# Kernel optimization log

Hardware: AMD Instinct MI355X
Metric: run time of the kernel (lower is better)

The kernel has to match this reference:

```python
import jax, jax.numpy as jnp
import numpy as np

B, C, H, W = 8, 512, 64, 64
TEMB = 512
HIDDEN = 1024  # int(C * prompt_hidden_ratio=2.0)
K = C // 2     # max(1, int(C * topk_ratio=0.5))


def silu(x):
    return x * jax.nn.sigmoid(x)


def conv1x1(h, w, b):
    # h: [b,c,hh,ww], w: [out,in], b: [out]
    return jnp.einsum('bchw,oc->bohw', h, w) + b[None, :, None, None]


def setup_inputs() -> dict:
    key = jax.random.key(0)
    ks = jax.random.split(key, 12)
    s = 0.02  # small init so softmax/attention stay well-conditioned
    return {
        'x': jax.random.normal(ks[0], (B, C, H, W), jnp.float32),
        'temb': jax.random.normal(ks[1], (B, TEMB), jnp.float32),
        'w_affine': jax.random.normal(ks[2], (2 * C, TEMB), jnp.float32) * s,
        'b_affine': jnp.zeros((2 * C,), jnp.float32),
        'w_tp': jax.random.normal(ks[3], (C, TEMB), jnp.float32) * s,
        'b_tp': jnp.zeros((C,), jnp.float32),
        'w_m1': jax.random.normal(ks[4], (HIDDEN, 2 * C), jnp.float32) * s,
        'b_m1': jnp.zeros((HIDDEN,), jnp.float32),
        'w_m2': jax.random.normal(ks[5], (C, HIDDEN), jnp.float32) * s,
        'b_m2': jnp.zeros((C,), jnp.float32),
        'wq': jax.random.normal(ks[6], (C, C), jnp.float32) * s,
        'bq': jnp.zeros((C,), jnp.float32),
        'wk': jax.random.normal(ks[7], (C, C), jnp.float32) * s,
        'bk': jnp.zeros((C,), jnp.float32),
        'wv': jax.random.normal(ks[8], (C, C), jnp.float32) * s,
        'bv': jnp.zeros((C,), jnp.float32),
        'wo': jax.random.normal(ks[9], (C, C), jnp.float32) * s,
        'bo': jnp.zeros((C,), jnp.float32),
    }


def reference(x, temb, w_affine, b_affine, w_tp, b_tp, w_m1, b_m1, w_m2, b_m2,
              wq, bq, wk, bk, wv, bv, wo, bo):
    b, c, hgt, wgt = x.shape
    hw = hgt * wgt

    # TimeScaleShift
    temb_act = silu(temb)
    ss = temb_act @ w_affine.T + b_affine              # [b, 2c]
    scale, shift = jnp.split(ss, 2, axis=1)
    h = x * (1.0 + scale[:, :, None, None]) + shift[:, :, None, None]

    # channel prompt
    gap = h.mean(axis=(2, 3))                          # [b, c]
    time_prompt = temb_act @ w_tp.T + b_tp             # [b, c]
    pm = jnp.concatenate([gap, time_prompt], axis=1)   # [b, 2c]
    prompt = silu(pm @ w_m1.T + b_m1) @ w_m2.T + b_m2  # [b, c]

    # top-k channel selection
    _, topk_idx = jax.lax.top_k(prompt, K)             # [b, K] int32

    # q/k/v 1x1 convs, then gather selected channels
    qf = conv1x1(h, wq, bq).reshape(b, c, hw)
    kf = conv1x1(h, wk, bk).reshape(b, c, hw)
    vf = conv1x1(h, wv, bv).reshape(b, c, hw)
    idx3 = topk_idx[:, :, None]
    q = jnp.take_along_axis(qf, idx3, axis=1)          # [b, K, hw]
    k_feat = jnp.take_along_axis(kf, idx3, axis=1)
    v = jnp.take_along_axis(vf, idx3, axis=1)

    # channel attention on the selected subset
    attn = jnp.einsum('bkn,bln->bkl', q, k_feat) * (K ** -0.5)  # [b, K, K]
    attn = jax.nn.softmax(attn, axis=2)
    out = jnp.einsum('bkl,bln->bkn', attn, v)                   # [b, K, hw]

    # scatter back into a zero tensor at the selected channels
    out_full = jax.vmap(
        lambda o, i: jnp.zeros((c, hw), o.dtype).at[i].set(o)
    )(out, topk_idx).reshape(b, c, hgt, wgt)

    return conv1x1(out_full, wo, bo)
```

## Files before the change

kernel.cpp:

```cpp
#include <hip/hip_runtime.h>
#include <hip/hip_bf16.h>
#include <math.h>

typedef __hip_bfloat16 bf16;
typedef __bf16 bf16x8 __attribute__((ext_vector_type(8)));
typedef float f32x4 __attribute__((ext_vector_type(4)));

static __device__ __forceinline__ float b2f(bf16 v) { return __bfloat162float(v); }
static __device__ __forceinline__ bf16 f2b(float v) { return __float2bfloat16(v); }

#define GLOAD16(g, l) __builtin_amdgcn_global_load_lds( \
    (const __attribute__((address_space(1))) void*)(g), \
    (__attribute__((address_space(3))) void*)(l), 16, 0, 0)

template <typename TOUT, int KSL>
__global__ __launch_bounds__(256) void gemm_ws(
    const bf16* __restrict__ A, size_t sA, int lda,
    const bf16* __restrict__ Bt, size_t sB, int ldb,
    const float* __restrict__ bias, size_t sBias, int hasBias,
    TOUT* __restrict__ D, size_t sD, size_t sDs,
    int N, int NMT, int NNC)
{
    constexpr int KSTEPS = KSL / 32;
    const int id = blockIdx.x;
    const int bz = id & 7;
    int slot = id >> 3;
    const int mt = slot % NMT; slot /= NMT;
    const int nc = slot % NNC;
    const int ks = slot / NNC;
    const int n0 = nc * 256;

    A  += (size_t)bz * sA + (size_t)(mt * 32) * lda + (size_t)ks * KSL;
    Bt += (size_t)bz * sB + (size_t)ks * KSL;
    D  += (size_t)bz * sD + (size_t)ks * sDs;
    if (hasBias) bias += (size_t)bz * sBias + mt * 32;

    const int t = threadIdx.x, wv = t >> 6, lane = t & 63;
    const int lr = lane & 15, quad = lane >> 4;
    const int xr7 = lr & 7;

    __shared__ bf16 lA[32 * KSL];

    if constexpr (KSL == 512) {
#pragma unroll
        for (int rr = 0; rr < 8; ++rr) {
            const int r = wv * 8 + rr;
            GLOAD16(A + (size_t)r * lda + ((lane ^ (r & 7)) << 3), &lA[r * 512]);
        }
    } else {
#pragma unroll
        for (int rr = 0; rr < 4; ++rr) {
            const int rb = wv * 8 + rr * 2;
            const int rl = rb + (lane >> 5);
            GLOAD16(A + (size_t)rl * lda + (((lane & 31) ^ (rl & 7)) << 3),
                    &lA[rb * 256]);
        }
    }
    __syncthreads();

    f32x4 acc[2][4];
#pragma unroll
    for (int i = 0; i < 2; ++i)
#pragma unroll
        for (int j = 0; j < 4; ++j) acc[i][j] = (f32x4){0.f, 0.f, 0.f, 0.f};

    const bf16* bp[4];
#pragma unroll
    for (int j = 0; j < 4; ++j)
        bp[j] = Bt + (size_t)(n0 + wv * 64 + j * 16 + lr) * ldb + quad * 8;

#pragma unroll 2
    for (int k2 = 0; k2 < KSTEPS; ++k2) {
        const int ao = ((((k2 << 2) | quad) ^ xr7) << 3);
        bf16x8 bfr[4];
#pragma unroll
        for (int j = 0; j < 4; ++j)
            bfr[j] = *(const bf16x8*)(bp[j] + k2 * 32);
        bf16x8 af0 = *(const bf16x8*)&lA[lr * KSL + ao];
        bf16x8 af1 = *(const bf16x8*)&lA[(16 + lr) * KSL + ao];
#pragma unroll
        for (int j = 0; j < 4; ++j) {
            acc[0][j] = __builtin_amdgcn_mfma_f32_16x16x32_bf16(af0, bfr[j], acc[0][j], 0, 0, 0);
            acc[1][j] = __builtin_amdgcn_mfma_f32_16x16x32_bf16(af1, bfr[j], acc[1][j], 0, 0, 0);
        }
    }

#pragma unroll
    for (int i = 0; i < 2; ++i) {
#pragma unroll
        for (int r = 0; r < 4; ++r) {
            const int ml = i * 16 + quad * 4 + r;
            const int mrow = mt * 32 + ml;
            const float bvv = hasBias ? bias[ml] : 0.f;
#pragma unroll
            for (int j = 0; j < 4; ++j) {
                const int nn = n0 + wv * 64 + j * 16 + lr;
                const float v = acc[i][j][r] + bvv;
                if constexpr (__is_same(TOUT, float)) D[(size_t)mrow * N + nn] = v;
                else                                  D[(size_t)mrow * N + nn] = f2b(v);
            }
        }
    }
}

__global__ __launch_bounds__(512, 4) void gemm_qkv3(
    const bf16* __restrict__ Aall, const bf16* __restrict__ xT,
    const float* __restrict__ bias,
    bf16* __restrict__ qb, bf16* __restrict__ kb, bf16* __restrict__ vT)
{
    const int id = blockIdx.x;
    const int b = id & 7;
    const int slot = id >> 3;
    const int mt = slot % 12;
    const int n0 = (slot / 12) * 512;

    const bf16* A  = Aall + (size_t)b * 393216 + (size_t)(mt * 64) * 512;
    const bf16* Bt = xT + (size_t)b * 2097152;
    bias += b * 768 + mt * 64;

    const int t = threadIdx.x, w = t >> 6, lane = t & 63;
    const int lr = lane & 15, quad = lane >> 4;
    const int xr7 = lr & 7;

    __shared__ bf16 lA[64 * 512];

#pragma unroll
    for (int rr = 0; rr < 8; ++rr) {
        const int r = w * 8 + rr;
        GLOAD16(A + (size_t)r * 512 + ((lane ^ (r & 7)) << 3), &lA[r * 512]);
    }
    __syncthreads();

    f32x4 acc[4][4];
#pragma unroll
    for (int i = 0; i < 4; ++i)
#pragma unroll
        for (int j = 0; j < 4; ++j) acc[i][j] = (f32x4){0.f, 0.f, 0.f, 0.f};

    const bf16* bp0 = Bt + (size_t)(n0 + w * 64 + lr) * 512 + quad * 8;

    for (int k2 = 0; k2 < 16; ++k2) {
        const int ao = ((((k2 << 2) | quad) ^ xr7) << 3);
        bf16x8 bfr[4];
#pragma unroll
        for (int j = 0; j < 4; ++j)
            bfr[j] = *(const bf16x8*)(bp0 + (size_t)j * 8192 + k2 * 32);
        bf16x8 af[4];
#pragma unroll
        for (int i = 0; i < 4; ++i)
            af[i] = *(const bf16x8*)&lA[(i * 16 + lr) * 512 + ao];
#pragma unroll
        for (int i = 0; i < 4; ++i)
#pragma unroll
            for (int j = 0; j < 4; ++j)
                acc[i][j] = __builtin_amdgcn_mfma_f32_16x16x32_bf16(af[i], bfr[j], acc[i][j], 0, 0, 0);
    }

#pragma unroll
    for (int i = 0; i < 4; ++i) {
#pragma unroll
        for (int r = 0; r < 4; ++r) {
            const int ml = i * 16 + quad * 4 + r;
            const int mmg = mt * 64 + ml;
            const int mloc = mmg & 255;
            const float bvv = bias[ml];
#pragma unroll
            for (int j = 0; j < 4; ++j) {
                const int nn = n0 + w * 64 + j * 16 + lr;
                const float v = acc[i][j][r] + bvv;
                if (mt < 4)       qb[(size_t)b * 1048576 + (size_t)mloc * 4096 + nn] = f2b(v);
                else if (mt < 8)  kb[(size_t)b * 1048576 + (size_t)mloc * 4096 + nn] = f2b(v);
                else              vT[(size_t)b * 1048576 + (size_t)nn * 256 + mloc] = f2b(v);
            }
        }
    }
}

__global__ __launch_bounds__(256) void k_prep(const float* __restrict__ x,
                                              bf16* __restrict__ xT,
                                              float* __restrict__ xsump)
{
    const int b = blockIdx.z;
    const int c0 = blockIdx.y * 64;
    const int n0 = blockIdx.x * 512;
    const int t = threadIdx.x;
    const int cr = t >> 2;
    const int sub = t & 3;
    __shared__ bf16 tile[64][72];

    const float* xrow = x + ((size_t)b * 512 + c0 + cr) * 4096 + n0 + sub * 16;
    float s = 0.f;

    for (int st = 0; st < 8; ++st) {
        __syncthreads();
        float4 f[4];
#pragma unroll
        for (int q = 0; q < 4; ++q) f[q] = *(const float4*)(xrow + st * 64 + q * 4);
#pragma unroll
        for (int q = 0; q < 4; ++q) {
            s += f[q].x + f[q].y + f[q].z + f[q].w;
            union { bf16 h[4]; uint2 u; } p;
            p.h[0] = f2b(f[q].x); p.h[1] = f2b(f[q].y);
            p.h[2] = f2b(f[q].z); p.h[3] = f2b(f[q].w);
            *(uint2*)&tile[cr][sub * 16 + q * 4] = p.u;
        }
        __syncthreads();
        union { bf16 h[8]; uint4 u; } o0, o1;
#pragma unroll
        for (int i = 0; i < 8; ++i) o0.h[i] = tile[sub * 16 + i][cr];
#pragma unroll
        for (int i = 0; i < 8; ++i) o1.h[i] = tile[sub * 16 + 8 + i][cr];
        bf16* orow = xT + ((size_t)b * 4096 + n0 + st * 64 + cr) * 512 + c0 + sub * 16;
        *(uint4*)(orow)     = o0.u;
        *(uint4*)(orow + 8) = o1.u;
    }
    s += __shfl_down(s, 2);
    s += __shfl_down(s, 1);
    if (sub == 0) xsump[(size_t)blockIdx.x * 4096 + b * 512 + c0 + cr] = s;
}


__global__ void k_smallgemm(const float* __restrict__ in, const float* __restrict__ W,
                            const float* __restrict__ bias, float* __restrict__ out,
                            int Mrows, int O, int Kd, int act, int inAct)
{
    const int gw = (blockIdx.x * 256 + threadIdx.x) >> 6;
    const int lane = threadIdx.x & 63;
    if (gw >= Mrows * O) return;
    const int m = gw / O, o = gw - m * O;
    float s = 0.f;
    for (int k = lane; k < Kd; k += 64) {
        float iv = in[m * Kd + k];
        if (inAct) iv = iv / (1.f + expf(-iv));
        s += iv * W[(size_t)o * Kd + k];
    }
    for (int off = 32; off; off >>= 1) s += __shfl_down(s, off);
    if (lane == 0) {
        s += bias[o];
        if (act) s = s / (1.f + expf(-s));
        out[m * O + o] = s;
    }
}

__global__ void k_mlp1(const float* __restrict__ ss, const float* __restrict__ xsump,
                       const float* __restrict__ tp, const float* __restrict__ w_m1,
                       const float* __restrict__ b_m1, float* __restrict__ hidden)
{
    const int gw = (blockIdx.x * 256 + threadIdx.x) >> 6;
    const int lane = threadIdx.x & 63;
    if (gw >= 8 * 1024) return;
    const int m = gw >> 10, o = gw & 1023;
    float s = 0.f;
    for (int k = lane; k < 1024; k += 64) {
        float pv;
        if (k < 512) {
            float xs = 0.f;
#pragma unroll
            for (int p = 0; p < 8; ++p) xs += xsump[p * 4096 + m * 512 + k];
            pv = (1.f + ss[m * 1024 + k]) * (xs * (1.f / 4096.f))
                 + ss[m * 1024 + 512 + k];
        } else {
            pv = tp[m * 512 + k - 512];
        }
        s += pv * w_m1[(size_t)o * 1024 + k];
    }
    for (int off = 32; off; off >>= 1) s += __shfl_down(s, off);
    if (lane == 0) {
        s += b_m1[o];
        hidden[m * 1024 + o] = s / (1.f + expf(-s));
    }
}

__global__ void k_topk(const float* __restrict__ prompt, int* __restrict__ idx)
{
    __shared__ float v[512];
    __shared__ int sel[512];
    const int b = blockIdx.x, c = threadIdx.x;
    v[c] = prompt[b * 512 + c];
    __syncthreads();
    const float mv = v[c];
    int rank = 0;
    for (int j = 0; j < 512; ++j) {
        float o = v[j];
        rank += (o > mv) || (o == mv && j < c);
    }
    sel[c] = (rank < 256) ? 1 : 0;
    __syncthreads();
    if (rank < 256) {
        int pos = 0;
        for (int j = 0; j < c; ++j) pos += sel[j];
        idx[b * 256 + pos] = c;
    }
}

__global__ void k_gather(const int* __restrict__ idx, const float* __restrict__ ss,
                         const float* __restrict__ wq, const float* __restrict__ wk,
                         const float* __restrict__ wv, const float* __restrict__ wo,
                         bf16* __restrict__ wqkv_g, bf16* __restrict__ wo_g)
{
    const int b = blockIdx.z;
    const int* id = idx + b * 256;
    const int tid = blockIdx.x * 256 + threadIdx.x;
    {
        const int mat = tid >> 17, r = tid & 131071;
        const int j = r >> 9, c = r & 511;
        const int ch = id[j];
        const float* W = mat == 0 ? wq : (mat == 1 ? wk : wv);
        wqkv_g[(size_t)b * 393216 + tid] = f2b(W[ch * 512 + c] * (1.f + ss[b * 1024 + c]));
    }
    if (tid < 131072) {
        const int o = tid >> 8, j = tid & 255;
        wo_g[(size_t)b * 131072 + tid] = f2b(wo[o * 512 + id[j]]);
    }
}

__global__ void k_biasadj(const int* __restrict__ idx, const float* __restrict__ ss,
                          const float* __restrict__ wq, const float* __restrict__ bq,
                          const float* __restrict__ wk, const float* __restrict__ bk,
                          const float* __restrict__ wv, const float* __restrict__ bv,
                          float* __restrict__ bqkv)
{
    const int gw = (blockIdx.x * 256 + threadIdx.x) >> 6;
    const int lane = threadIdx.x & 63;
    if (gw >= 8 * 768) return;
    const int b = gw / 768, j3 = gw - b * 768;
    const int mat = j3 >> 8, j = j3 & 255;
    const int ch = idx[b * 256 + j];
    const float* W  = mat == 0 ? wq : (mat == 1 ? wk : wv);
    const float* Bb = mat == 0 ? bq : (mat == 1 ? bk : bv);
    const float* shift = ss + b * 1024 + 512;
    float s = 0.f;
    for (int c = lane; c < 512; c += 64)
        s += W[(size_t)ch * 512 + c] * shift[c];
    for (int off = 32; off; off >>= 1) s += __shfl_down(s, off);
    if (lane == 0) bqkv[b * 768 + j3] = Bb[ch] + s;
}

__global__ void k_softmax_red(const float* __restrict__ part, bf16* __restrict__ Pt)
{
    const int row = blockIdx.x;
    const int b = row >> 8, j = row & 255;
    const int t = threadIdx.x;
    const int lane = t & 63, wv = t >> 6;
    __shared__ float redm[4], reds[4];
    float v = 0.f;
#pragma unroll
    for (int s = 0; s < 8; ++s)
        v += part[((size_t)(s * 8 + b) * 256 + j) * 256 + t];
    v *= 0.0625f;
    float m = v;
    for (int off = 32; off; off >>= 1) m = fmaxf(m, __shfl_down(m, off));
    if (lane == 0) redm[wv] = m;
    __syncthreads();
    m = fmaxf(fmaxf(redm[0], redm[1]), fmaxf(redm[2], redm[3]));
    const float e = __expf(v - m);
    float s = e;
    for (int off = 32; off; off >>= 1) s += __shfl_down(s, off);
    if (lane == 0) reds[wv] = s;
    __syncthreads();
    s = reds[0] + reds[1] + reds[2] + reds[3];
    Pt[(size_t)b * 65536 + (size_t)t * 256 + j] = f2b(e / s);
}


extern "C" void kernel_launch(void* const* d_in, const int* in_sizes, int n_in,
                              void* d_out, int out_size, void* d_ws, size_t ws_size,
                              hipStream_t stream)
{
    const float* x        = (const float*)d_in[0];
    const float* temb     = (const float*)d_in[1];
    const float* w_affine = (const float*)d_in[2];
    const float* b_affine = (const float*)d_in[3];
    const float* w_tp     = (const float*)d_in[4];
    const float* b_tp     = (const float*)d_in[5];
    const float* w_m1     = (const float*)d_in[6];
    const float* b_m1     = (const float*)d_in[7];
    const float* w_m2     = (const float*)d_in[8];
    const float* b_m2     = (const float*)d_in[9];
    const float* wq       = (const float*)d_in[10];
    const float* bq       = (const float*)d_in[11];
    const float* wk       = (const float*)d_in[12];
    const float* bk       = (const float*)d_in[13];
    const float* wv       = (const float*)d_in[14];
    const float* bv       = (const float*)d_in[15];
    const float* wo       = (const float*)d_in[16];
    const float* bo       = (const float*)d_in[17];
    float* out = (float*)d_out;

    char* ws = (char*)d_ws;
    size_t off = 0;
    auto alloc = [&](size_t bytes) -> char* {
        char* p = ws + off;
        off += (bytes + 255) & ~(size_t)255;
        return p;
    };

    float* ssb      = (float*)alloc(8192 * 4);
    float* tp       = (float*)alloc(4096 * 4);
    float* xsump    = (float*)alloc((size_t)8 * 4096 * 4);
    float* hidden   = (float*)alloc(8192 * 4);
    float* prompt   = (float*)alloc(4096 * 4);
    int*   idx      = (int*)alloc(2048 * 4);
    bf16*  xT     = (bf16*)alloc((size_t)8 * 4096 * 512 * 2);
    float* part   = (float*)alloc((size_t)8 * 8 * 256 * 256 * 4);
    bf16*  wqkv_g = (bf16*)alloc((size_t)8 * 768 * 512 * 2);
    float* bqkv_g = (float*)alloc(8 * 768 * 4);
    bf16*  wo_g   = (bf16*)alloc((size_t)8 * 512 * 256 * 2);
    bf16*  qb     = (bf16*)alloc((size_t)8 * 256 * 4096 * 2);
    bf16*  kb     = (bf16*)alloc((size_t)8 * 256 * 4096 * 2);
    bf16*  vT     = (bf16*)alloc((size_t)8 * 4096 * 256 * 2);
    bf16*  Pt     = (bf16*)alloc((size_t)8 * 256 * 256 * 2);
    bf16*  W2     = (bf16*)alloc((size_t)8 * 512 * 256 * 2);
    (void)ws_size; (void)n_in; (void)in_sizes; (void)out_size;

    k_prep<<<dim3(8, 8, 8), 256, 0, stream>>>(x, xT, xsump);
    k_smallgemm<<<2048, 256, 0, stream>>>(temb, w_affine, b_affine, ssb, 8, 1024, 512, 0, 1);
    k_smallgemm<<<1024, 256, 0, stream>>>(temb, w_tp, b_tp, tp, 8, 512, 512, 0, 1);
    k_mlp1<<<2048, 256, 0, stream>>>(ssb, xsump, tp, w_m1, b_m1, hidden);
    k_smallgemm<<<1024, 256, 0, stream>>>(hidden, w_m2, b_m2, prompt, 8, 512, 1024, 0, 0);
    k_topk<<<8, 512, 0, stream>>>(prompt, idx);
    k_gather<<<dim3(1536, 1, 8), 256, 0, stream>>>(idx, ssb, wq, wk, wv, wo, wqkv_g, wo_g);
    k_biasadj<<<1536, 256, 0, stream>>>(idx, ssb, wq, bq, wk, bk, wv, bv, bqkv_g);

    gemm_qkv3<<<768, 512, 0, stream>>>(wqkv_g, xT, bqkv_g, qb, kb, vT);

    gemm_ws<float, 512><<<512, 256, 0, stream>>>(
        qb, 1048576, 4096, kb, 1048576, 4096,
        nullptr, 0, 0,
        part, 65536, 524288, 256, 8, 1);

    k_softmax_red<<<2048, 256, 0, stream>>>(part, Pt);

    gemm_ws<bf16, 256><<<128, 256, 0, stream>>>(
        wo_g, 131072, 256, Pt, 65536, 256,
        nullptr, 0, 0,
        W2, 131072, 0, 256, 16, 1);

    gemm_ws<float, 256><<<2048, 256, 0, stream>>>(
        W2, 131072, 256, vT, 1048576, 256,
        bo, 0, 1,
        out, 2097152, 0, 4096, 16, 16);
}
```

Baseline: 394.2 us.

## Reformulate channel attention via Gram matrix of x and fold weights algebraically

Instead of materialising q, k, v feature maps per batch, the attention logits are computed from the per-batch Gram matrix x·xᵀ (512x512), modulated by scale/shift corrections, then projected through the gathered Wq/Wk. The output projection Wo·attn·Wv is collapsed into a single 512x512 per-batch matrix applied to x, with bias terms folded into a per-channel constant. A new pipelined triple-buffered GEMM kernel replaces the previous GEMMs. This removes the large qkv GEMM and its memory traffic at the cost of an extra bf16 copy of x and more small kernels, with some precision risk from bf16 Gram accumulation.

```diff
diff --git a/kernel.cpp b/kernel.cpp
--- a/kernel.cpp
+++ b/kernel.cpp
@@ -13,172 +13,107 @@
     (const __attribute__((address_space(1))) void*)(g), \
     (__attribute__((address_space(3))) void*)(l), 16, 0, 0)
 
-template <typename TOUT, int KSL>
-__global__ __launch_bounds__(256) void gemm_ws(
+#define WAITVM(N) asm volatile("s_waitcnt vmcnt(" #N ")" ::: "memory")
+
+#define TM 128
+#define TN 64
+#define TK 32
+
+template <typename TOUT>
+__global__ __launch_bounds__(256) void gemm_bt2(
     const bf16* __restrict__ A, size_t sA, int lda,
     const bf16* __restrict__ Bt, size_t sB, int ldb,
     const float* __restrict__ bias, size_t sBias, int hasBias,
-    TOUT* __restrict__ D, size_t sD, size_t sDs,
-    int N, int NMT, int NNC)
-{
-    constexpr int KSTEPS = KSL / 32;
+    TOUT* __restrict__ D, size_t sD, size_t sDk,
+    int M, int N, int kLen, int transStore, int NXB, int NYB)
+{
     const int id = blockIdx.x;
     const int bz = id & 7;
     int slot = id >> 3;
-    const int mt = slot % NMT; slot /= NMT;
-    const int nc = slot % NNC;
-    const int ks = slot / NNC;
-    const int n0 = nc * 256;
-
-    A  += (size_t)bz * sA + (size_t)(mt * 32) * lda + (size_t)ks * KSL;
-    Bt += (size_t)bz * sB + (size_t)ks * KSL;
-    D  += (size_t)bz * sD + (size_t)ks * sDs;
-    if (hasBias) bias += (size_t)bz * sBias + mt * 32;
-
+    const int bx = slot % NXB; slot /= NXB;
+    const int by = slot % NYB;
+    const int ks = slot / NYB;
+
+    A  += (size_t)bz * sA + (size_t)ks * kLen;
+    Bt += (size_t)bz * sB + (size_t)ks * kLen;
+    D  += (size_t)bz * sD + (size_t)ks * sDk;
+    if (hasBias) bias += (size_t)bz * sBias;
+
+    const int m0 = by * TM, n0 = bx * TN;
     const int t = threadIdx.x, wv = t >> 6, lane = t & 63;
     const int lr = lane & 15, quad = lane >> 4;
-    const int xr7 = lr & 7;
-
-    __shared__ bf16 lA[32 * KSL];
-
-    if constexpr (KSL == 512) {
-#pragma unroll
-        for (int rr = 0; rr < 8; ++rr) {
-            const int r = wv * 8 + rr;
-            GLOAD16(A + (size_t)r * lda + ((lane ^ (r & 7)) << 3), &lA[r * 512]);
+    const int qx8 = (quad ^ ((lr >> 1) & 3)) * 8;
+
+    __shared__ bf16 lA[3][TM * TK];
+    __shared__ bf16 lB[3][TN * TK];
+
+    f32x4 acc[2][4];
+#pragma unroll
+    for (int i = 0; i < 2; ++i)
+#pragma unroll
+        for (int j = 0; j < 4; ++j) acc[i][j] = (f32x4){0.f, 0.f, 0.f, 0.f};
+
+    const int srow = lane >> 2;
+    const int scol = ((lane & 3) ^ ((lane >> 3) & 3)) * 8;
+    const bf16* as0 = A  + (size_t)(m0 + wv * 16 + srow) * lda + scol;
+    const bf16* bs0 = Bt + (size_t)(n0 + wv * 16 + srow) * ldb + scol;
+
+    GLOAD16(as0, &lA[0][wv * 512]);
+    GLOAD16(as0 + (size_t)64 * lda, &lA[0][wv * 512 + 2048]);
+    GLOAD16(bs0, &lB[0][wv * 512]);
+    GLOAD16(as0 + TK, &lA[1][wv * 512]);
+    GLOAD16(as0 + (size_t)64 * lda + TK, &lA[1][wv * 512 + 2048]);
+    GLOAD16(bs0 + TK, &lB[1][wv * 512]);
+    WAITVM(3);
+    __builtin_amdgcn_s_barrier();
+
+    int cur = 0;
+    for (int k0 = 0; k0 < kLen; k0 += TK) {
+        int kn = k0 + 2 * TK; if (kn >= kLen) kn -= kLen;
+        int nx2 = cur + 2; if (nx2 >= 3) nx2 -= 3;
+        GLOAD16(as0 + kn, &lA[nx2][wv * 512]);
+        GLOAD16(as0 + (size_t)64 * lda + kn, &lA[nx2][wv * 512 + 2048]);
+        GLOAD16(bs0 + kn, &lB[nx2][wv * 512]);
+
+        const bf16* bA = lA[cur];
+        const bf16* bB = lB[cur];
+        bf16x8 af0 = *(const bf16x8*)(bA + (wv * 32 + lr) * 32 + qx8);
+        bf16x8 af1 = *(const bf16x8*)(bA + (wv * 32 + 16 + lr) * 32 + qx8);
+#pragma unroll
+        for (int j = 0; j < 4; ++j) {
+            bf16x8 bfj = *(const bf16x8*)(bB + (j * 16 + lr) * 32 + qx8);
+            acc[0][j] = __builtin_amdgcn_mfma_f32_16x16x32_bf16(af0, bfj, acc[0][j], 0, 0, 0);
+            acc[1][j] = __builtin_amdgcn_mfma_f32_16x16x32_bf16(af1, bfj, acc[1][j], 0, 0, 0);
         }
-    } else {
-#pragma unroll
-        for (int rr = 0; rr < 4; ++rr) {
-            const int rb = wv * 8 + rr * 2;
-            const int rl = rb + (lane >> 5);
-            GLOAD16(A + (size_t)rl * lda + (((lane & 31) ^ (rl & 7)) << 3),
-                    &lA[rb * 256]);
-        }
-    }
-    __syncthreads();
-
-    f32x4 acc[2][4];
-#pragma unroll
-    for (int i = 0; i < 2; ++i)
-#pragma unroll
-        for (int j = 0; j < 4; ++j) acc[i][j] = (f32x4){0.f, 0.f, 0.f, 0.f};
-
-    const bf16* bp[4];
-#pragma unroll
-    for (int j = 0; j < 4; ++j)
-        bp[j] = Bt + (size_t)(n0 + wv * 64 + j * 16 + lr) * ldb + quad * 8;
-
-#pragma unroll 2
-    for (int k2 = 0; k2 < KSTEPS; ++k2) {
-        const int ao = ((((k2 << 2) | quad) ^ xr7) << 3);
-        bf16x8 bfr[4];
-#pragma unroll
-        for (int j = 0; j < 4; ++j)
-            bfr[j] = *(const bf16x8*)(bp[j] + k2 * 32);
-        bf16x8 af0 = *(const bf16x8*)&lA[lr * KSL + ao];
-        bf16x8 af1 = *(const bf16x8*)&lA[(16 + lr) * KSL + ao];
-#pragma unroll
-        for (int j = 0; j < 4; ++j) {
-            acc[0][j] = __builtin_amdgcn_mfma_f32_16x16x32_bf16(af0, bfr[j], acc[0][j], 0, 0, 0);
-            acc[1][j] = __builtin_amdgcn_mfma_f32_16x16x32_bf16(af1, bfr[j], acc[1][j], 0, 0, 0);
-        }
+        WAITVM(3);
+        __builtin_amdgcn_s_barrier();
+        cur = (cur + 1 == 3) ? 0 : cur + 1;
     }
 
 #pragma unroll
     for (int i = 0; i < 2; ++i) {
+        const int mb = m0 + wv * 32 + i * 16 + quad * 4;
 #pragma unroll
         for (int r = 0; r < 4; ++r) {
-            const int ml = i * 16 + quad * 4 + r;
-            const int mrow = mt * 32 + ml;
-            const float bvv = hasBias ? bias[ml] : 0.f;
+            const int mm = mb + r;
+            const float bvv = hasBias ? bias[mm] : 0.f;
 #pragma unroll
             for (int j = 0; j < 4; ++j) {
-                const int nn = n0 + wv * 64 + j * 16 + lr;
+                const int nn = n0 + j * 16 + lr;
                 const float v = acc[i][j][r] + bvv;
-                if constexpr (__is_same(TOUT, float)) D[(size_t)mrow * N + nn] = v;
-                else                                  D[(size_t)mrow * N + nn] = f2b(v);
+                const size_t o = transStore ? ((size_t)nn * M + mm)
+                                            : ((size_t)mm * N + nn);
+                if constexpr (__is_same(TOUT, float)) D[o] = v;
+                else                                  D[o] = f2b(v);
             }
         }
     }
 }
 
-__global__ __launch_bounds__(512, 4) void gemm_qkv3(
-    const bf16* __restrict__ Aall, const bf16* __restrict__ xT,
-    const float* __restrict__ bias,
-    bf16* __restrict__ qb, bf16* __restrict__ kb, bf16* __restrict__ vT)
-{
-    const int id = blockIdx.x;
-    const int b = id & 7;
-    const int slot = id >> 3;
-    const int mt = slot % 12;
-    const int n0 = (slot / 12) * 512;
-
-    const bf16* A  = Aall + (size_t)b * 393216 + (size_t)(mt * 64) * 512;
-    const bf16* Bt = xT + (size_t)b * 2097152;
-    bias += b * 768 + mt * 64;
-
-    const int t = threadIdx.x, w = t >> 6, lane = t & 63;
-    const int lr = lane & 15, quad = lane >> 4;
-    const int xr7 = lr & 7;
-
-    __shared__ bf16 lA[64 * 512];
-
-#pragma unroll
-    for (int rr = 0; rr < 8; ++rr) {
-        const int r = w * 8 + rr;
-        GLOAD16(A + (size_t)r * 512 + ((lane ^ (r & 7)) << 3), &lA[r * 512]);
-    }
-    __syncthreads();
-
-    f32x4 acc[4][4];
-#pragma unroll
-    for (int i = 0; i < 4; ++i)
-#pragma unroll
-        for (int j = 0; j < 4; ++j) acc[i][j] = (f32x4){0.f, 0.f, 0.f, 0.f};
-
-    const bf16* bp0 = Bt + (size_t)(n0 + w * 64 + lr) * 512 + quad * 8;
-
-    for (int k2 = 0; k2 < 16; ++k2) {
-        const int ao = ((((k2 << 2) | quad) ^ xr7) << 3);
-        bf16x8 bfr[4];
-#pragma unroll
-        for (int j = 0; j < 4; ++j)
-            bfr[j] = *(const bf16x8*)(bp0 + (size_t)j * 8192 + k2 * 32);
-        bf16x8 af[4];
-#pragma unroll
-        for (int i = 0; i < 4; ++i)
-            af[i] = *(const bf16x8*)&lA[(i * 16 + lr) * 512 + ao];
-#pragma unroll
-        for (int i = 0; i < 4; ++i)
-#pragma unroll
-            for (int j = 0; j < 4; ++j)
-                acc[i][j] = __builtin_amdgcn_mfma_f32_16x16x32_bf16(af[i], bfr[j], acc[i][j], 0, 0, 0);
-    }
-
-#pragma unroll
-    for (int i = 0; i < 4; ++i) {
-#pragma unroll
-        for (int r = 0; r < 4; ++r) {
-            const int ml = i * 16 + quad * 4 + r;
-            const int mmg = mt * 64 + ml;
-            const int mloc = mmg & 255;
-            const float bvv = bias[ml];
-#pragma unroll
-            for (int j = 0; j < 4; ++j) {
-                const int nn = n0 + w * 64 + j * 16 + lr;
-                const float v = acc[i][j][r] + bvv;
-                if (mt < 4)       qb[(size_t)b * 1048576 + (size_t)mloc * 4096 + nn] = f2b(v);
-                else if (mt < 8)  kb[(size_t)b * 1048576 + (size_t)mloc * 4096 + nn] = f2b(v);
-                else              vT[(size_t)b * 1048576 + (size_t)nn * 256 + mloc] = f2b(v);
-            }
-        }
-    }
-}
-
-__global__ __launch_bounds__(256) void k_prep(const float* __restrict__ x,
-                                              bf16* __restrict__ xT,
-                                              float* __restrict__ xsump)
+__global__ __launch_bounds__(256) void k_prep2(const float* __restrict__ x,
+                                               bf16* __restrict__ xb,
+                                               bf16* __restrict__ xT,
+                                               float* __restrict__ xsump)
 {
     const int b = blockIdx.z;
     const int c0 = blockIdx.y * 64;
@@ -188,7 +123,9 @@
     const int sub = t & 3;
     __shared__ bf16 tile[64][72];
 
-    const float* xrow = x + ((size_t)b * 512 + c0 + cr) * 4096 + n0 + sub * 16;
+    const size_t rowoff = ((size_t)b * 512 + c0 + cr) * 4096 + n0 + sub * 16;
+    const float* xrow = x + rowoff;
+    bf16* xbrow = xb + rowoff;
     float s = 0.f;
 
     for (int st = 0; st < 8; ++st) {
@@ -196,14 +133,16 @@
         float4 f[4];
 #pragma unroll
         for (int q = 0; q < 4; ++q) f[q] = *(const float4*)(xrow + st * 64 + q * 4);
+        union { bf16 h[16]; uint4 u[2]; } pk;
 #pragma unroll
         for (int q = 0; q < 4; ++q) {
             s += f[q].x + f[q].y + f[q].z + f[q].w;
-            union { bf16 h[4]; uint2 u; } p;
-            p.h[0] = f2b(f[q].x); p.h[1] = f2b(f[q].y);
-            p.h[2] = f2b(f[q].z); p.h[3] = f2b(f[q].w);
-            *(uint2*)&tile[cr][sub * 16 + q * 4] = p.u;
+            pk.h[q * 4 + 0] = f2b(f[q].x); pk.h[q * 4 + 1] = f2b(f[q].y);
+            pk.h[q * 4 + 2] = f2b(f[q].z); pk.h[q * 4 + 3] = f2b(f[q].w);
+            *(uint2*)&tile[cr][sub * 16 + q * 4] = *(uint2*)&pk.h[q * 4];
         }
+        *(uint4*)(xbrow + st * 64)     = pk.u[0];
+        *(uint4*)(xbrow + st * 64 + 8) = pk.u[1];
         __syncthreads();
         union { bf16 h[8]; uint4 u; } o0, o1;
 #pragma unroll
@@ -293,73 +232,147 @@
     }
 }
 
-__global__ void k_gather(const int* __restrict__ idx, const float* __restrict__ ss,
-                         const float* __restrict__ wq, const float* __restrict__ wk,
-                         const float* __restrict__ wv, const float* __restrict__ wo,
-                         bf16* __restrict__ wqkv_g, bf16* __restrict__ wo_g)
+__global__ void k_mod(const float* __restrict__ ssb, const float* __restrict__ xsump,
+                      float* __restrict__ smod, float* __restrict__ shm,
+                      float* __restrict__ xst, float* __restrict__ rsh)
+{
+    const int g = blockIdx.x * 256 + threadIdx.x;
+    if (g >= 4096) return;
+    const int b = g >> 9, c = g & 511;
+    float xs = 0.f;
+#pragma unroll
+    for (int p = 0; p < 8; ++p) xs += xsump[p * 4096 + b * 512 + c];
+    const float sm = 1.f + ssb[b * 1024 + c];
+    const float sh = ssb[b * 1024 + 512 + c];
+    smod[g] = sm; shm[g] = sh; xst[g] = xs;
+    rsh[g] = sm * xs + 4096.f * sh;
+}
+
+__global__ void k_gather2(const int* __restrict__ idx,
+                          const float* __restrict__ wq, const float* __restrict__ wk,
+                          const float* __restrict__ wv, const float* __restrict__ wo,
+                          const float* __restrict__ bq, const float* __restrict__ bk,
+                          const float* __restrict__ bv,
+                          bf16* __restrict__ Wqg, bf16* __restrict__ Wkg,
+                          bf16* __restrict__ WvT, bf16* __restrict__ wog,
+                          float* __restrict__ bqg, float* __restrict__ bkg,
+                          float* __restrict__ bvg)
 {
     const int b = blockIdx.z;
     const int* id = idx + b * 256;
     const int tid = blockIdx.x * 256 + threadIdx.x;
     {
-        const int mat = tid >> 17, r = tid & 131071;
-        const int j = r >> 9, c = r & 511;
+        const int j = tid >> 9, c = tid & 511;
         const int ch = id[j];
-        const float* W = mat == 0 ? wq : (mat == 1 ? wk : wv);
-        wqkv_g[(size_t)b * 393216 + tid] = f2b(W[ch * 512 + c] * (1.f + ss[b * 1024 + c]));
-    }
-    if (tid < 131072) {
-        const int o = tid >> 8, j = tid & 255;
-        wo_g[(size_t)b * 131072 + tid] = f2b(wo[o * 512 + id[j]]);
-    }
-}
-
-__global__ void k_biasadj(const int* __restrict__ idx, const float* __restrict__ ss,
-                          const float* __restrict__ wq, const float* __restrict__ bq,
-                          const float* __restrict__ wk, const float* __restrict__ bk,
-                          const float* __restrict__ wv, const float* __restrict__ bv,
-                          float* __restrict__ bqkv)
+        Wqg[(size_t)b * 131072 + tid] = f2b(wq[(size_t)ch * 512 + c]);
+        Wkg[(size_t)b * 131072 + tid] = f2b(wk[(size_t)ch * 512 + c]);
+    }
+    {
+        const int c = tid >> 8, j = tid & 255;
+        const int ch = id[j];
+        WvT[(size_t)b * 131072 + tid] = f2b(wv[(size_t)ch * 512 + c]);
+        wog[(size_t)b * 131072 + tid] = f2b(wo[(size_t)(tid >> 8) * 512 + id[j]]);
+    }
+    if (tid < 256) {
+        const int ch = id[tid];
+        bqg[b * 256 + tid] = bq[ch];
+        bkg[b * 256 + tid] = bk[ch];
+        bvg[b * 256 + tid] = bv[ch];
+    }
+}
+
+__global__ void k_vecs(const int* __restrict__ idx, const float* __restrict__ rsh,
+                       const float* __restrict__ wq, const float* __restrict__ wk,
+                       float* __restrict__ qrow, float* __restrict__ krow)
 {
     const int gw = (blockIdx.x * 256 + threadIdx.x) >> 6;
     const int lane = threadIdx.x & 63;
-    if (gw >= 8 * 768) return;
-    const int b = gw / 768, j3 = gw - b * 768;
-    const int mat = j3 >> 8, j = j3 & 255;
-    const int ch = idx[b * 256 + j];
-    const float* W  = mat == 0 ? wq : (mat == 1 ? wk : wv);
-    const float* Bb = mat == 0 ? bq : (mat == 1 ? bk : bv);
-    const float* shift = ss + b * 1024 + 512;
+    if (gw >= 8 * 512) return;
+    const int b = gw >> 9, r = gw & 511;
+    const int i = r & 255, sel = r >> 8;
+    const int ch = idx[b * 256 + i];
+    const float* W = sel ? wk : wq;
     float s = 0.f;
     for (int c = lane; c < 512; c += 64)
-        s += W[(size_t)ch * 512 + c] * shift[c];
+        s += W[(size_t)ch * 512 + c] * rsh[b * 512 + c];
     for (int off = 32; off; off >>= 1) s += __shfl_down(s, off);
-    if (lane == 0) bqkv[b * 768 + j3] = Bb[ch] + s;
-}
-
-__global__ void k_softmax_red(const float* __restrict__ part, bf16* __restrict__ Pt)
+    if (lane == 0) (sel ? krow : qrow)[b * 256 + i] = s;
+}
+
+__global__ void k_gmod(const float* __restrict__ part,
+                       const float* __restrict__ smod, const float* __restrict__ shm,
+                       const float* __restrict__ xst, bf16* __restrict__ G)
+{
+    const int b = blockIdx.x >> 9, c = blockIdx.x & 511;
+    const float sc = smod[b * 512 + c], hc = shm[b * 512 + c], xc = xst[b * 512 + c];
+#pragma unroll
+    for (int h = 0; h < 2; ++h) {
+        const int d = threadIdx.x + h * 256;
+        const size_t o = (size_t)b * 262144 + (size_t)c * 512 + d;
+        float g = part[o] + part[2097152 + o];
+        const float sd = smod[b * 512 + d], hd = shm[b * 512 + d], xd = xst[b * 512 + d];
+        G[o] = f2b(sc * sd * g + sc * hd * xc + sd * hc * xd + 4096.f * hc * hd);
+    }
+}
+
+__global__ void k_soft2(const float* __restrict__ S0,
+                        const float* __restrict__ qrow, const float* __restrict__ krow,
+                        const float* __restrict__ bqg, const float* __restrict__ bkg,
+                        const float* __restrict__ bvg,
+                        bf16* __restrict__ attn, float* __restrict__ ew)
 {
     const int row = blockIdx.x;
-    const int b = row >> 8, j = row & 255;
+    const int b = row >> 8, i = row & 255;
     const int t = threadIdx.x;
-    const int lane = t & 63, wv = t >> 6;
-    __shared__ float redm[4], reds[4];
-    float v = 0.f;
-#pragma unroll
-    for (int s = 0; s < 8; ++s)
-        v += part[((size_t)(s * 8 + b) * 256 + j) * 256 + t];
-    v *= 0.0625f;
+    const int lane = t & 63, wvi = t >> 6;
+    __shared__ float redm[4], reds[4], rede[4];
+    const float bqi = bqg[b * 256 + i], qri = qrow[b * 256 + i];
+    float v = S0[(size_t)b * 65536 + (size_t)i * 256 + t];
+    v = (v + bqi * krow[b * 256 + t] + qri * bkg[b * 256 + t]
+           + 4096.f * bqi * bkg[b * 256 + t]) * 0.0625f;
     float m = v;
     for (int off = 32; off; off >>= 1) m = fmaxf(m, __shfl_down(m, off));
-    if (lane == 0) redm[wv] = m;
+    if (lane == 0) redm[wvi] = m;
     __syncthreads();
     m = fmaxf(fmaxf(redm[0], redm[1]), fmaxf(redm[2], redm[3]));
     const float e = __expf(v - m);
     float s = e;
     for (int off = 32; off; off >>= 1) s += __shfl_down(s, off);
-    if (lane == 0) reds[wv] = s;
+    if (lane == 0) reds[wvi] = s;
     __syncthreads();
     s = reds[0] + reds[1] + reds[2] + reds[3];
-    Pt[(size_t)b * 65536 + (size_t)t * 256 + j] = f2b(e / s);
+    const float a = e / s;
+    attn[(size_t)b * 65536 + (size_t)i * 256 + t] = f2b(a);
+    float ev = a * bvg[b * 256 + t];
+    for (int off = 32; off; off >>= 1) ev += __shfl_down(ev, off);
+    if (lane == 0) rede[wvi] = ev;
+    __syncthreads();
+    if (t == 0) ew[b * 256 + i] = rede[0] + rede[1] + rede[2] + rede[3];
+}
+
+__global__ void k_m2x(const float* __restrict__ Mmat, const float* __restrict__ smod,
+                      const float* __restrict__ shm, const bf16* __restrict__ wog,
+                      const float* __restrict__ ew, const float* __restrict__ bo,
+                      bf16* __restrict__ M2, float* __restrict__ c1)
+{
+    const int b = blockIdx.x >> 9, o = blockIdx.x & 511;
+    const int t = threadIdx.x;
+    const int lane = t & 63, wvi = t >> 6;
+    __shared__ float red[4];
+    float p = 0.f;
+#pragma unroll
+    for (int h = 0; h < 2; ++h) {
+        const int c = t + h * 256;
+        const size_t off = (size_t)b * 262144 + (size_t)o * 512 + c;
+        const float mv = Mmat[off];
+        M2[off] = f2b(mv * smod[b * 512 + c]);
+        p += mv * shm[b * 512 + c];
+    }
+    p += b2f(wog[(size_t)b * 131072 + (size_t)o * 256 + t]) * ew[b * 256 + t];
+    for (int off = 32; off; off >>= 1) p += __shfl_down(p, off);
+    if (lane == 0) red[wvi] = p;
+    __syncthreads();
+    if (t == 0) c1[b * 512 + o] = red[0] + red[1] + red[2] + red[3] + bo[o];
 }
 
 
@@ -395,49 +408,86 @@
         return p;
     };
 
-    float* ssb      = (float*)alloc(8192 * 4);
-    float* tp       = (float*)alloc(4096 * 4);
-    float* xsump    = (float*)alloc((size_t)8 * 4096 * 4);
-    float* hidden   = (float*)alloc(8192 * 4);
-    float* prompt   = (float*)alloc(4096 * 4);
-    int*   idx      = (int*)alloc(2048 * 4);
+    float* ssb    = (float*)alloc(8192 * 4);
+    float* tp     = (float*)alloc(4096 * 4);
+    float* xsump  = (float*)alloc((size_t)8 * 4096 * 4);
+    float* hidden = (float*)alloc(8192 * 4);
+    float* prompt = (float*)alloc(4096 * 4);
+    int*   idx    = (int*)alloc(2048 * 4);
+    float* smod   = (float*)alloc(4096 * 4);
+    float* shm    = (float*)alloc(4096 * 4);
+    float* xst    = (float*)alloc(4096 * 4);
+    float* rsh    = (float*)alloc(4096 * 4);
+    float* qrow   = (float*)alloc(2048 * 4);
+    float* krow   = (float*)alloc(2048 * 4);
+    float* bqg    = (float*)alloc(2048 * 4);
+    float* bkg    = (float*)alloc(2048 * 4);
+    float* bvg    = (float*)alloc(2048 * 4);
+    float* ew     = (float*)alloc(2048 * 4);
+    float* c1     = (float*)alloc(4096 * 4);
+    bf16*  xb     = (bf16*)alloc((size_t)8 * 512 * 4096 * 2);
     bf16*  xT     = (bf16*)alloc((size_t)8 * 4096 * 512 * 2);
-    float* part   = (float*)alloc((size_t)8 * 8 * 256 * 256 * 4);
-    bf16*  wqkv_g = (bf16*)alloc((size_t)8 * 768 * 512 * 2);
-    float* bqkv_g = (float*)alloc(8 * 768 * 4);
-    bf16*  wo_g   = (bf16*)alloc((size_t)8 * 512 * 256 * 2);
-    bf16*  qb     = (bf16*)alloc((size_t)8 * 256 * 4096 * 2);
-    bf16*  kb     = (bf16*)alloc((size_t)8 * 256 * 4096 * 2);
-    bf16*  vT     = (bf16*)alloc((size_t)8 * 4096 * 256 * 2);
-    bf16*  Pt     = (bf16*)alloc((size_t)8 * 256 * 256 * 2);
-    bf16*  W2     = (bf16*)alloc((size_t)8 * 512 * 256 * 2);
+    bf16*  G      = (bf16*)alloc((size_t)8 * 512 * 512 * 2);
+    bf16*  Wqg    = (bf16*)alloc((size_t)8 * 256 * 512 * 2);
+    bf16*  Wkg    = (bf16*)alloc((size_t)8 * 256 * 512 * 2);
+    bf16*  WvT    = (bf16*)alloc((size_t)8 * 512 * 256 * 2);
+    bf16*  wog    = (bf16*)alloc((size_t)8 * 512 * 256 * 2);
+    char*  uni  = alloc((size_t)20 * 1024 * 1024);
+    float* part = (float*)uni;
+    bf16*  T    = (bf16*)uni;
+    bf16*  attn = (bf16*)(uni + 2097152);
+    bf16*  Ut   = (bf16*)(uni + 3145728);
+    float* S0   = (float*)(uni + 5242880);
+    float* Mmat = (float*)(uni + 7340032);
+    bf16*  M2   = (bf16*)(uni + 15728640);
     (void)ws_size; (void)n_in; (void)in_sizes; (void)out_size;
 
-    k_prep<<<dim3(8, 8, 8), 256, 0, stream>>>(x, xT, xsump);
+    k_prep2<<<dim3(8, 8, 8), 256, 0, stream>>>(x, xb, xT, xsump);
+
+    gemm_bt2<float><<<512, 256, 0, stream>>>(
+        xb, 2097152, 4096, xb, 2097152, 4096,
+        nullptr, 0, 0,
+        part, 262144, 2097152, 512, 512, 2048, 0, 8, 4);
+
     k_smallgemm<<<2048, 256, 0, stream>>>(temb, w_affine, b_affine, ssb, 8, 1024, 512, 0, 1);
     k_smallgemm<<<1024, 256, 0, stream>>>(temb, w_tp, b_tp, tp, 8, 512, 512, 0, 1);
+    k_mod<<<16, 256, 0, stream>>>(ssb, xsump, smod, shm, xst, rsh);
     k_mlp1<<<2048, 256, 0, stream>>>(ssb, xsump, tp, w_m1, b_m1, hidden);
     k_smallgemm<<<1024, 256, 0, stream>>>(hidden, w_m2, b_m2, prompt, 8, 512, 1024, 0, 0);
     k_topk<<<8, 512, 0, stream>>>(prompt, idx);
-    k_gather<<<dim3(1536, 1, 8), 256, 0, stream>>>(idx, ssb, wq, wk, wv, wo, wqkv_g, wo_g);
-    k_biasadj<<<1536, 256, 0, stream>>>(idx, ssb, wq, bq, wk, bk, wv, bv, bqkv_g);
-
-    gemm_qkv3<<<768, 512, 0, stream>>>(wqkv_g, xT, bqkv_g, qb, kb, vT);
-
-    gemm_ws<float, 512><<<512, 256, 0, stream>>>(
-        qb, 1048576, 4096, kb, 1048576, 4096,
+
+    k_gather2<<<dim3(512, 1, 8), 256, 0, stream>>>(idx, wq, wk, wv, wo, bq, bk, bv,
+                                                   Wqg, Wkg, WvT, wog, bqg, bkg, bvg);
+    k_vecs<<<1024, 256, 0, stream>>>(idx, rsh, wq, wk, qrow, krow);
+
+    k_gmod<<<4096, 256, 0, stream>>>(part, smod, shm, xst, G);
+
+    gemm_bt2<bf16><<<128, 256, 0, stream>>>(
+        Wqg, 131072, 512, G, 262144, 512,
         nullptr, 0, 0,
-        part, 65536, 524288, 256, 8, 1);
-
-    k_softmax_red<<<2048, 256, 0, stream>>>(part, Pt);
-
-    gemm_ws<bf16, 256><<<128, 256, 0, stream>>>(
-        wo_g, 131072, 256, Pt, 65536, 256,
+        T, 131072, 0, 256, 512, 512, 0, 8, 2);
+
+    gemm_bt2<float><<<64, 256, 0, stream>>>(
+        T, 131072, 512, Wkg, 131072, 512,
         nullptr, 0, 0,
-        W2, 131072, 0, 256, 16, 1);
-
-    gemm_ws<float, 256><<<2048, 256, 0, stream>>>(
-        W2, 131072, 256, vT, 1048576, 256,
-        bo, 0, 1,
-        out, 2097152, 0, 4096, 16, 16);
-}
+        S0, 65536, 0, 256, 256, 512, 0, 4, 2);
+
+    k_soft2<<<2048, 256, 0, stream>>>(S0, qrow, krow, bqg, bkg, bvg, attn, ew);
+
+    gemm_bt2<bf16><<<128, 256, 0, stream>>>(
+        attn, 65536, 256, WvT, 131072, 256,
+        nullptr, 0, 0,
+        Ut, 131072, 0, 256, 512, 256, 1, 8, 2);
+
+    gemm_bt2<float><<<256, 256, 0, stream>>>(
+        wog, 131072, 256, Ut, 131072, 256,
+        nullptr, 0, 0,
+        Mmat, 262144, 0, 512, 512, 256, 0, 8, 4);
+
+    k_m2x<<<4096, 256, 0, stream>>>(Mmat, smod, shm, wog, ew, bo, M2, c1);
+
+    gemm_bt2<float><<<2048, 256, 0, stream>>>(
+        M2, 262144, 512, xT, 2097152, 512,
+        c1, 512, 1,
+        out, 2097152, 0, 512, 4096, 512, 0, 64, 4);
+}
```

Measured after the change: 367.3 us. -6.8%, faster.
